# Kernel optimization log

Hardware: AMD Instinct MI355X
Metric: run time of the kernel (lower is better)

## Reference

```python
import jax, jax.numpy as jnp
import numpy as np

B = 16
NT, NH_, NW_, T_, H_, W_ = 4, 14, 14, 4, 1, 1
C = 768
NHEAD = 12
HD = C // NHEAD
SCALE = 1.0 / float(np.sqrt(HD))
TT = NT * T_            # 16 temporal slices
T2 = TT // 2            # 8 after even/odd split
HW = (NH_ * H_) * (NW_ * W_)  # 196 spatial tokens
TOKENS = NT * NH_ * NW_ * T_ * H_ * W_


def setup_inputs() -> dict:
    key = jax.random.key(0)
    ks = jax.random.split(key, 14)
    def lin(k, din, dout):
        return jax.random.normal(k, (din, dout), jnp.float32) * 0.02
    return {
        "x_in": jax.random.normal(ks[0], (B, TOKENS, C), jnp.float32),
        "Wq_d": lin(ks[1], C, C),      "bq_d": jnp.zeros((C,), jnp.float32),
        "Wkv_a": lin(ks[2], C, 2 * C), "bkv_a": jnp.zeros((2 * C,), jnp.float32),
        "Wq_a": lin(ks[3], C, C),      "bq_a": jnp.zeros((C,), jnp.float32),
        "Wkv_d": lin(ks[4], C, 2 * C), "bkv_d": jnp.zeros((2 * C,), jnp.float32),
        "Wp_d": lin(ks[5], C, C),      "bp_d": jnp.zeros((C,), jnp.float32),
        "Wp_a": lin(ks[6], C, C),      "bp_a": jnp.zeros((C,), jnp.float32),
    }


def _cross_attn(q_x, kv_x, Wq, bq, Wkv, bkv):
    # q_x, kv_x: (b, t, hw, c)
    b, t, hw, c = q_x.shape
    q = (q_x @ Wq + bq).reshape(b, t, hw, NHEAD, HD)
    kv = (kv_x @ Wkv + bkv).reshape(b, t, hw, 2, NHEAD, HD)
    k, v = kv[..., 0, :, :], kv[..., 1, :, :]
    s = jnp.einsum('btqhd,btkhd->bthqk', q, k) * SCALE
    p = jax.nn.softmax(s, axis=-1)
    o = jnp.einsum('bthqk,btkhd->btqhd', p, v)
    return o.reshape(b, t, hw, c)


def reference(x_in, Wq_d, bq_d, Wkv_a, bkv_a, Wq_a, bq_a, Wkv_d, bkv_d,
              Wp_d, bp_d, Wp_a, bp_a):
    b = x_in.shape[0]
    # einops: b (nt nh nw t h w) c -> b (nt t) (nh h) (nw w) c
    x = x_in.reshape(b, NT, NH_, NW_, T_, H_, W_, C)
    x = x.transpose(0, 1, 4, 2, 5, 3, 6, 7).reshape(b, TT, NH_ * H_, NW_ * W_, C)
    x_skip = x                                   # (b, TT, h, w, c)
    x = x.reshape(b, TT, HW, C)                  # (b, TT, hw, c)
    x_a = x[:, 0::2]                             # (b, T2, hw, c) approx
    x_d = x[:, 1::2]                             # (b, T2, hw, c) detail

    # detail cross-attends to approx, subtract-update
    _d = _cross_attn(x_d, x_a, Wq_d, bq_d, Wkv_a, bkv_a)
    _d = jax.nn.gelu(_d @ Wp_d + bp_d, approximate=False)
    x_d = x_d - _d
    # approx cross-attends to updated detail, add-update
    _a = _cross_attn(x_a, x_d, Wq_a, bq_a, Wkv_d, bkv_d)
    _a = jax.nn.gelu(_a @ Wp_a + bp_a, approximate=False)
    x_a = x_a + _a

    # relaxed_constrain: pooled-skip minus channel-mean of x_a
    xs = x_skip.reshape(b, TT, HW, C)
    pooled = xs.reshape(b, T2, 2, HW, C).mean(axis=2)   # avg_pool2d (2,1)
    pool_a = pooled.mean(axis=-1) - x_a.mean(axis=-1)   # (b, T2, hw)

    # SSL=False: mean over channels, keepdim (torch layout b,1,t,hw)
    x_d_out = x_d.mean(axis=-1)[:, None, :, :]          # (b, 1, T2, hw)
    return (pool_a, x_d_out)
```

## Files before the change

kernel.cpp:

```cpp
#include <hip/hip_runtime.h>

typedef __bf16 bf16;
typedef __attribute__((ext_vector_type(8))) __bf16 bf16x8;
typedef __attribute__((ext_vector_type(4))) __bf16 bf16x4;
typedef __attribute__((ext_vector_type(2))) __bf16 bf16x2;
typedef __attribute__((ext_vector_type(4))) float f32x4;
typedef __attribute__((ext_vector_type(4))) unsigned int u32x4;

#define TOKENS 3136
#define CC 768
#define S196 196
#define M_ROWS 25088
#define BATCH 16

__device__ __forceinline__ float bf2f(bf16 x) { return (float)x; }
__device__ __forceinline__ bf16 f2bf(float x) { return (bf16)x; }

__device__ __forceinline__ float gelu_exact(float x) {
    return 0.5f * x * (1.0f + erff(x * 0.70710678118654752f));
}

__device__ __forceinline__ unsigned int packbf(float a, float b) {
    bf16x2 v; v[0] = (bf16)a; v[1] = (bf16)b;
    return __builtin_bit_cast(unsigned int, v);
}

#define GLOAD_LDS16(gp, lp) \
    __builtin_amdgcn_global_load_lds((const __attribute__((address_space(1))) void*)(gp), \
                                     (__attribute__((address_space(3))) void*)(lp), 16, 0, 0)

__global__ __launch_bounds__(256)
void transpose_w(const float* __restrict__ W, bf16* __restrict__ Wt, int K, int N)
{
    __shared__ float tle[32][33];
    int k0 = blockIdx.x * 32, n0 = blockIdx.y * 32;
    int tx = threadIdx.x & 31, ty = threadIdx.x >> 5;
    for (int r = ty; r < 32; r += 8)
        tle[r][tx] = W[(long)(k0 + r) * N + n0 + tx];
    __syncthreads();
    for (int r = ty; r < 32; r += 8)
        Wt[(long)(n0 + r) * K + k0 + tx] = f2bf(tle[tx][r]);
}

__global__ __launch_bounds__(256)
void conv_bias(const float* b0, const float* b1, const float* b2,
               const float* b3, const float* b4, const float* b5,
               bf16* __restrict__ dst)
{
    const float* srcs[6] = {b0, b1, b2, b3, b4, b5};
    const int sizes[6]   = {768, 1536, 768, 1536, 768, 768};
    const int offs[6]    = {0, 768, 2304, 3072, 4608, 5376};
    int which = blockIdx.x;
    const float* s = srcs[which];
    int n = sizes[which];
    bf16* d = dst + offs[which];
    for (int i = threadIdx.x; i < n; i += 256)
        d[i] = f2bf(s[i]);
}

__global__ __launch_bounds__(256)
void reorder_split(const float* __restrict__ x_in, bf16* __restrict__ xa,
                   bf16* __restrict__ xd)
{
    long idx = (long)blockIdx.x * 256 + threadIdx.x;
    const long total = (long)BATCH * 16 * S196 * 96;
    if (idx >= total) return;
    int  c8  = (int)(idx % 96) * 8;
    long row = idx / 96;
    int  s   = (int)(row % S196);
    long r2  = row / S196;
    int  tt  = (int)(r2 & 15);
    int  b   = (int)(r2 >> 4);
    int  nt  = tt >> 2, t = tt & 3;
    int  nh  = s / 14,  nw = s % 14;
    long src  = ((long)b * TOKENS + ((nt * 14 + nh) * 14 + nw) * 4 + t) * CC + c8;
    bf16* dst = (tt & 1) ? xd : xa;
    long doff = ((long)(b * 8 + (tt >> 1)) * S196 + s) * CC + c8;
    const float* sp = x_in + src;
    f32x4 a = *(const f32x4*)sp;
    f32x4 c = *(const f32x4*)(sp + 4);
    bf16x8 v;
    v[0] = f2bf(a[0]); v[1] = f2bf(a[1]); v[2] = f2bf(a[2]); v[3] = f2bf(a[3]);
    v[4] = f2bf(c[0]); v[5] = f2bf(c[1]); v[6] = f2bf(c[2]); v[7] = f2bf(c[3]);
    *(bf16x8*)(dst + doff) = v;
}

__device__ __forceinline__ float row_sum768(const bf16* __restrict__ p, int lane)
{
    float s = 0.f;
    bf16x8 v = *(const bf16x8*)(p + lane * 8);
    #pragma unroll
    for (int j = 0; j < 8; ++j) s += bf2f(v[j]);
    if (lane < 32) {
        bf16x8 w = *(const bf16x8*)(p + 512 + lane * 8);
        #pragma unroll
        for (int j = 0; j < 8; ++j) s += bf2f(w[j]);
    }
    #pragma unroll
    for (int off = 32; off; off >>= 1) s += __shfl_xor(s, off, 64);
    return s;
}

__global__ __launch_bounds__(256)
void pool_ad(const bf16* __restrict__ xa, const bf16* __restrict__ xd,
             float* __restrict__ pool0)
{
    int id = blockIdx.x * 4 + (threadIdx.x >> 6);
    int lane = threadIdx.x & 63;
    float sa = row_sum768(xa + (long)id * CC, lane);
    float sd = row_sum768(xd + (long)id * CC, lane);
    if (lane == 0) pool0[id] = (sa + sd) * (0.5f / 768.0f);
}

__global__ __launch_bounds__(256)
void out_final(const bf16* __restrict__ xa, const bf16* __restrict__ xd,
               const float* __restrict__ pool0, float* __restrict__ out)
{
    int id = blockIdx.x * 4 + (threadIdx.x >> 6);
    int lane = threadIdx.x & 63;
    float sa = row_sum768(xa + (long)id * CC, lane);
    float sd = row_sum768(xd + (long)id * CC, lane);
    if (lane == 0) {
        out[id]          = pool0[id] - sa * (1.0f / 768.0f);
        out[M_ROWS + id] = sd * (1.0f / 768.0f);
    }
}

template<int EPI>
__global__ __launch_bounds__(256)
void gemm_bt128(const bf16* __restrict__ A, const bf16* __restrict__ Bt,
                const bf16* __restrict__ bias, const bf16* __restrict__ res,
                bf16* __restrict__ C, int ldc, int K, int mTiles, int nTiles)
{
    constexpr int BM = 128, BK = 32;
    __shared__ alignas(16) bf16 sA[BM * BK];
    __shared__ alignas(16) bf16 sB[BM * BK];
    const int tid  = threadIdx.x;
    const int lane = tid & 63, wave = tid >> 6;
    const int wm   = wave >> 1, wn = wave & 1;
    const int quad = lane >> 4, l16 = lane & 15;

    const int GM = 16;
    int pid   = blockIdx.x;
    int group = GM * nTiles;
    int gid   = pid / group;
    int rem   = pid - gid * group;
    int first = gid * GM;
    int gm    = (mTiles - first < GM) ? (mTiles - first) : GM;
    int bm    = first + rem % gm;
    int bn    = rem / gm;

    const long m0 = (long)bm * BM;
    const long n0 = (long)bn * BM;

    f32x4 acc[4][4] = {};

    for (int kt = 0; kt < K; kt += BK) {
        if (kt) __syncthreads();
        #pragma unroll
        for (int c = 0; c < 2; ++c) {
            int ci = (wave * 2 + c) * 64 + lane;
            int r  = ci >> 2, kc = ci & 3;
            const bf16* ga = A  + (m0 + r) * K + kt + kc * 8;
            const bf16* gb = Bt + (n0 + r) * K + kt + kc * 8;
            bf16* la = sA + (wave * 2 + c) * 512;
            bf16* lb = sB + (wave * 2 + c) * 512;
            GLOAD_LDS16(ga, la);
            GLOAD_LDS16(gb, lb);
        }
        __syncthreads();

        bf16x8 af[4], bfr[4];
        #pragma unroll
        for (int mi = 0; mi < 4; ++mi)
            af[mi] = *(const bf16x8*)(sA + (wm * 64 + mi * 16 + l16) * BK + quad * 8);
        #pragma unroll
        for (int ni = 0; ni < 4; ++ni)
            bfr[ni] = *(const bf16x8*)(sB + (wn * 64 + ni * 16 + l16) * BK + quad * 8);
        #pragma unroll
        for (int mi = 0; mi < 4; ++mi)
            #pragma unroll
            for (int ni = 0; ni < 4; ++ni)
                acc[mi][ni] = __builtin_amdgcn_mfma_f32_16x16x32_bf16(af[mi], bfr[ni], acc[mi][ni], 0, 0, 0);
    }

    #pragma unroll
    for (int mi = 0; mi < 4; ++mi) {
        #pragma unroll
        for (int ni = 0; ni < 4; ++ni) {
            int mg = (int)m0 + wm * 64 + mi * 16 + quad * 4;
            int ng = (int)n0 + wn * 64 + ni * 16 + l16;
            float bn_ = bf2f(bias[ng]);
            #pragma unroll
            for (int r = 0; r < 4; ++r) {
                float x = acc[mi][ni][r] + bn_;
                long off = (long)(mg + r) * ldc + ng;
                if (EPI == 0)      C[off] = f2bf(x);
                else if (EPI == 1) C[off] = f2bf(bf2f(res[off]) - gelu_exact(x));
                else               C[off] = f2bf(bf2f(res[off]) + gelu_exact(x));
            }
        }
    }
}

template<int EPI>
__global__ __launch_bounds__(512, 2)
void gemm_bt256(const bf16* __restrict__ A, const bf16* __restrict__ Bt,
                const bf16* __restrict__ bias, const bf16* __restrict__ res,
                bf16* __restrict__ C, int ldc, int mTiles, int nTiles)
{
    constexpr int K = 768, NKT = 12;
    __shared__ alignas(16) bf16 sA[4][8192];
    __shared__ alignas(16) bf16 sB[4][8192];
    const int tid  = threadIdx.x;
    const int lane = tid & 63, wave = tid >> 6;
    const int wm   = wave >> 2, wn = wave & 3;
    const int quad = lane >> 4, l16 = lane & 15;

    int nwg  = (int)gridDim.x;
    int orig = (int)blockIdx.x;
    int q8 = nwg >> 3, r8 = nwg & 7, xcd = orig & 7;
    int pid = (xcd < r8 ? xcd * (q8 + 1) : r8 * (q8 + 1) + (xcd - r8) * q8)
              + (orig >> 3);

    const int GM = 8;
    int group = GM * nTiles;
    int gid   = pid / group;
    int rem   = pid - gid * group;
    int first = gid * GM;
    int gm    = (mTiles - first < GM) ? (mTiles - first) : GM;
    int bm    = first + rem % gm;
    int bn    = rem / gm;

    const long m0 = (long)bm * 256;
    const long n0 = (long)bn * 256;

    const int lh  = l16 >> 1;
    const int px  = ((l16 & 1) << 2) | quad;
    const int pxl = (px ^ lh) * 8;
    const int aoffA = (wm * 64 + lh) * 64 + pxl;
    const int aoffB = (wn * 32 + lh) * 64 + pxl;

    const int  cg  = (tid & 7) ^ ((tid >> 3) & 7);
    const int  rr  = ((tid >> 3) << 1) + (cg >> 2);
    const long soA0 = (long)rr * K + (cg & 3) * 8;
    const long soA1 = (long)(128 + rr) * K + (cg & 3) * 8;
    const int  ldd0 = wave * 512, ldd1 = 4096 + wave * 512;
    const bf16* Ab = A  + m0 * K;
    const bf16* Bb = Bt + n0 * K;

    f32x4 acc[8][4] = {};

    #define STG_A(slot, koff) do { \
        GLOAD_LDS16(Ab + (koff) + soA0, &sA[slot][ldd0]); \
        GLOAD_LDS16(Ab + (koff) + soA1, &sA[slot][ldd1]); } while (0)
    #define STG_B(slot, koff) do { \
        GLOAD_LDS16(Bb + (koff) + soA0, &sB[slot][ldd0]); \
        GLOAD_LDS16(Bb + (koff) + soA1, &sB[slot][ldd1]); } while (0)

    STG_A(0, 0);  STG_B(0, 0);
    STG_A(1, 32); STG_B(1, 32);
    STG_A(2, 64); STG_B(2, 64);
    asm volatile("s_waitcnt vmcnt(8)" ::: "memory");
    __builtin_amdgcn_s_barrier();

    #define MFMA16(H) do { \
        __builtin_amdgcn_s_setprio(1); \
        _Pragma("unroll") \
        for (int mf = 0; mf < 4; ++mf) \
            _Pragma("unroll") \
            for (int nf = 0; nf < 4; ++nf) \
                acc[(H)*4 + mf][nf] = __builtin_amdgcn_mfma_f32_16x16x32_bf16( \
                    a[mf], b[nf], acc[(H)*4 + mf][nf], 0, 0, 0); \
        __builtin_amdgcn_s_setprio(0); } while (0)

    #pragma unroll 2
    for (int t = 0; t < NKT; ++t) {
        const int sl0 = (2 * t) & 3;
        const int sl1 = (2 * t + 1) & 3;
        const int slN = (2 * t + 3) & 3;
        bf16x8 a[4], b[4];

        #pragma unroll
        for (int mf = 0; mf < 4; ++mf) a[mf] = *(const bf16x8*)(&sA[sl0][mf * 512 + aoffA]);
        #pragma unroll
        for (int nf = 0; nf < 4; ++nf) b[nf] = *(const bf16x8*)(&sB[sl0][nf * 512 + aoffB]);
        if (t + 1 < NKT) STG_A(slN, (t + 1) * 64 + 32);
        __builtin_amdgcn_s_barrier();
        MFMA16(0);
        __builtin_amdgcn_s_barrier();

        #pragma unroll
        for (int mf = 0; mf < 4; ++mf) a[mf] = *(const bf16x8*)(&sA[sl0][2048 + mf * 512 + aoffA]);
        if (t + 1 < NKT) STG_B(slN, (t + 1) * 64 + 32);
        __builtin_amdgcn_s_barrier();
        MFMA16(1);
        if (t + 1 < NKT) asm volatile("s_waitcnt vmcnt(8)" ::: "memory");
        else             asm volatile("s_waitcnt vmcnt(0)" ::: "memory");
        __builtin_amdgcn_s_barrier();

        #pragma unroll
        for (int mf = 0; mf < 4; ++mf) a[mf] = *(const bf16x8*)(&sA[sl1][mf * 512 + aoffA]);
        #pragma unroll
        for (int nf = 0; nf < 4; ++nf) b[nf] = *(const bf16x8*)(&sB[sl1][nf * 512 + aoffB]);
        if (t + 2 < NKT) STG_A(sl0, (t + 2) * 64);
        __builtin_amdgcn_s_barrier();
        MFMA16(0);
        __builtin_amdgcn_s_barrier();

        #pragma unroll
        for (int mf = 0; mf < 4; ++mf) a[mf] = *(const bf16x8*)(&sA[sl1][2048 + mf * 512 + aoffA]);
        if (t + 2 < NKT) STG_B(sl0, (t + 2) * 64);
        __builtin_amdgcn_s_barrier();
        MFMA16(1);
        if      (t + 2 < NKT) asm volatile("s_waitcnt vmcnt(8)" ::: "memory");
        else if (t + 1 < NKT) asm volatile("s_waitcnt vmcnt(4)" ::: "memory");
        __builtin_amdgcn_s_barrier();
    }
    #undef STG_A
    #undef STG_B
    #undef MFMA16

    #pragma unroll
    for (int mf = 0; mf < 8; ++mf) {
        #pragma unroll
        for (int nf = 0; nf < 4; ++nf) {
            int mg = (int)m0 + wm * 128 + mf * 16 + quad * 4;
            int ng = (int)n0 + wn * 64 + nf * 16 + l16;
            float bn_ = bf2f(bias[ng]);
            #pragma unroll
            for (int r = 0; r < 4; ++r) {
                float x = acc[mf][nf][r] + bn_;
                long off = (long)(mg + r) * ldc + ng;
                if (EPI == 0)      C[off] = f2bf(x);
                else if (EPI == 1) C[off] = f2bf(bf2f(res[off]) - gelu_exact(x));
                else               C[off] = f2bf(bf2f(res[off]) + gelu_exact(x));
            }
        }
    }
}

#define KSTR 72
#define VSTR 264

__global__ __launch_bounds__(256)
void attn_mfma(const bf16* __restrict__ Q, int ldq,
               const bf16* __restrict__ KV, int ldkv,
               bf16* __restrict__ O)
{
    const int h  = blockIdx.x;
    const int bj = blockIdx.y;
    __shared__ alignas(16) bf16 Ks[208 * KSTR];
    __shared__ alignas(16) bf16 Vt[64 * VSTR];
    const int tid = threadIdx.x, lane = tid & 63, wave = tid >> 6;
    const int quad = lane >> 4, l16 = lane & 15;

    const bf16* qg = Q  + (long)bj * S196 * ldq  + h * 64;
    const bf16* kg = KV + (long)bj * S196 * ldkv + h * 64;
    const bf16* vg = kg + CC;

    for (int i = tid; i < 208 * 8; i += 256) {
        int r = i >> 3, c8 = (i & 7) * 8;
        bf16x8 v = {};
        if (r < S196) v = *(const bf16x8*)(kg + (long)r * ldkv + c8);
        *(bf16x8*)(Ks + r * KSTR + c8) = v;
    }
    for (int i = tid; i < 256 * 8; i += 256) {
        int g   = i >> 6;
        int c8  = (g & 7) * 8;
        int tok = (g >> 3) * 64 + (i & 63);
        bf16x8 v = {};
        if (tok < S196) v = *(const bf16x8*)(vg + (long)tok * ldkv + c8);
        #pragma unroll
        for (int j = 0; j < 8; ++j)
            Vt[(c8 + j) * VSTR + tok] = v[j];
    }
    __syncthreads();

    for (int qt = wave; qt < 13; qt += 4) {
        int qrow = qt * 16 + l16; if (qrow > 195) qrow = 195;
        const bf16* qrp = qg + (long)qrow * ldq + quad * 8;
        bf16x8 qf0 = *(const bf16x8*)(qrp);
        bf16x8 qf1 = *(const bf16x8*)(qrp + 32);

        f32x4 st[13];
        #pragma unroll
        for (int rt = 0; rt < 13; ++rt) st[rt] = (f32x4){0.f, 0.f, 0.f, 0.f};
        #pragma unroll
        for (int rt = 0; rt < 13; ++rt) {
            const bf16* kb = Ks + (rt * 16 + l16) * KSTR + quad * 8;
            bf16x8 kf0 = *(const bf16x8*)(kb);
            bf16x8 kf1 = *(const bf16x8*)(kb + 32);
            st[rt] = __builtin_amdgcn_mfma_f32_16x16x32_bf16(kf0, qf0, st[rt], 0, 0, 0);
            st[rt] = __builtin_amdgcn_mfma_f32_16x16x32_bf16(kf1, qf1, st[rt], 0, 0, 0);
        }

        const float SC = 0.125f;
        #pragma unroll
        for (int rt = 0; rt < 13; ++rt) {
            st[rt][0] *= SC; st[rt][1] *= SC; st[rt][2] *= SC; st[rt][3] *= SC;
        }
        if (quad != 0)
            st[12] = (f32x4){-1e30f, -1e30f, -1e30f, -1e30f};

        float m = -1e30f;
        #pragma unroll
        for (int rt = 0; rt < 13; ++rt)
            m = fmaxf(m, fmaxf(fmaxf(st[rt][0], st[rt][1]), fmaxf(st[rt][2], st[rt][3])));
        m = fmaxf(m, __shfl_xor(m, 16, 64));
        m = fmaxf(m, __shfl_xor(m, 32, 64));
        float sum = 0.f;
        #pragma unroll
        for (int rt = 0; rt < 13; ++rt) {
            st[rt][0] = __expf(st[rt][0] - m);
            st[rt][1] = __expf(st[rt][1] - m);
            st[rt][2] = __expf(st[rt][2] - m);
            st[rt][3] = __expf(st[rt][3] - m);
            sum += st[rt][0] + st[rt][1] + st[rt][2] + st[rt][3];
        }
        sum += __shfl_xor(sum, 16, 64);
        sum += __shfl_xor(sum, 32, 64);
        float inv = 1.0f / sum;

        unsigned int pk[13][2];
        #pragma unroll
        for (int rt = 0; rt < 13; ++rt) {
            pk[rt][0] = packbf(st[rt][0] * inv, st[rt][1] * inv);
            pk[rt][1] = packbf(st[rt][2] * inv, st[rt][3] * inv);
        }

        f32x4 ot[4];
        #pragma unroll
        for (int dt = 0; dt < 4; ++dt) ot[dt] = (f32x4){0.f, 0.f, 0.f, 0.f};
        #pragma unroll
        for (int c = 0; c < 7; ++c) {
            u32x4 fp;
            #pragma unroll
            for (int jp = 0; jp < 4; ++jp) {
                int jh = jp >> 1, rp = jp & 1;
                int srcb = ((((quad & 1) << 1) + jh) << 6) | (l16 << 2);
                int a = __builtin_amdgcn_ds_bpermute(srcb, (int)pk[2 * c][rp]);
                int b = (c < 6) ? __builtin_amdgcn_ds_bpermute(srcb, (int)pk[2 * c + 1][rp]) : 0;
                fp[jp] = (quad >> 1) ? (unsigned int)b : (unsigned int)a;
            }
            bf16x8 pB = __builtin_bit_cast(bf16x8, fp);
            #pragma unroll
            for (int dt = 0; dt < 4; ++dt) {
                bf16x8 vf = *(const bf16x8*)(Vt + (dt * 16 + l16) * VSTR + c * 32 + quad * 8);
                ot[dt] = __builtin_amdgcn_mfma_f32_16x16x32_bf16(vf, pB, ot[dt], 0, 0, 0);
            }
        }

        int token = qt * 16 + l16;
        if (token < S196) {
            bf16* op = O + ((long)bj * S196 + token) * CC + h * 64 + quad * 4;
            #pragma unroll
            for (int dt = 0; dt < 4; ++dt) {
                bf16x4 v;
                v[0] = f2bf(ot[dt][0]); v[1] = f2bf(ot[dt][1]);
                v[2] = f2bf(ot[dt][2]); v[3] = f2bf(ot[dt][3]);
                *(bf16x4*)(op + dt * 16) = v;
            }
        }
    }
}

extern "C" void kernel_launch(void* const* d_in, const int* in_sizes, int n_in,
                              void* d_out, int out_size, void* d_ws, size_t ws_size,
                              hipStream_t stream)
{
    const float* x_in  = (const float*)d_in[0];
    const float* Wq_d  = (const float*)d_in[1];
    const float* bq_d  = (const float*)d_in[2];
    const float* Wkv_a = (const float*)d_in[3];
    const float* bkv_a = (const float*)d_in[4];
    const float* Wq_a  = (const float*)d_in[5];
    const float* bq_a  = (const float*)d_in[6];
    const float* Wkv_d = (const float*)d_in[7];
    const float* bkv_d = (const float*)d_in[8];
    const float* Wp_d  = (const float*)d_in[9];
    const float* bp_d  = (const float*)d_in[10];
    const float* Wp_a  = (const float*)d_in[11];
    const float* bp_a  = (const float*)d_in[12];
    float* out = (float*)d_out;

    char* w = (char*)d_ws;
    auto alloc = [&](size_t elems) {
        bf16* p = (bf16*)w;
        w += ((elems * 2 + 255) / 256) * 256;
        return p;
    };
    bf16* biasAll = alloc(6144);
    bf16* WtQd  = alloc((size_t)768 * 768);
    bf16* WtACat= alloc((size_t)2304 * 768);
    bf16* WtKd  = alloc((size_t)1536 * 768);
    bf16* WtPd  = alloc((size_t)768 * 768);
    bf16* WtPa  = alloc((size_t)768 * 768);
    bf16* xa    = alloc((size_t)M_ROWS * 768);
    bf16* xd    = alloc((size_t)M_ROWS * 768);
    bf16* Qb    = alloc((size_t)M_ROWS * 768);
    bf16* QKVa  = alloc((size_t)M_ROWS * 2304);
    bf16* Ob    = alloc((size_t)M_ROWS * 768);
    float* pool0 = (float*)w; w += ((size_t)M_ROWS * 4 + 255) / 256 * 256;

    dim3 blk(256);
    dim3 blk512(512);
    transpose_w<<<dim3(24, 24), blk, 0, stream>>>(Wq_d,  WtQd, 768, 768);
    transpose_w<<<dim3(24, 48), blk, 0, stream>>>(Wkv_a, WtACat, 768, 1536);
    transpose_w<<<dim3(24, 24), blk, 0, stream>>>(Wq_a,  WtACat + (size_t)1536 * 768, 768, 768);
    transpose_w<<<dim3(24, 48), blk, 0, stream>>>(Wkv_d, WtKd, 768, 1536);
    transpose_w<<<dim3(24, 24), blk, 0, stream>>>(Wp_d,  WtPd, 768, 768);
    transpose_w<<<dim3(24, 24), blk, 0, stream>>>(Wp_a,  WtPa, 768, 768);
    conv_bias<<<dim3(6), blk, 0, stream>>>(bq_d, bkv_a, bq_a, bkv_d, bp_d, bp_a, biasAll);

    long total_chunks = (long)BATCH * 16 * S196 * 96;
    int  rblocks = (int)((total_chunks + 255) / 256);
    reorder_split<<<rblocks, blk, 0, stream>>>(x_in, xa, xd);
    pool_ad<<<M_ROWS / 4, blk, 0, stream>>>(xa, xd, pool0);

    const bf16* Bq_d   = biasAll;
    const bf16* Bkva_qa= biasAll + 768;
    const bf16* Bkv_d  = biasAll + 3072;
    const bf16* Bp_d   = biasAll + 4608;
    const bf16* Bp_a   = biasAll + 5376;

    gemm_bt128<0><<<dim3(196 * 6), blk, 0, stream>>>(xd, WtQd, Bq_d, nullptr, Qb, 768, 768, 196, 6);
    gemm_bt256<0><<<dim3(98 * 9), blk512, 0, stream>>>(xa, WtACat, Bkva_qa, nullptr, QKVa, 2304, 98, 9);
    attn_mfma<<<dim3(12, 128), blk, 0, stream>>>(Qb, 768, QKVa, 2304, Ob);
    gemm_bt128<1><<<dim3(196 * 6), blk, 0, stream>>>(Ob, WtPd, Bp_d, xd, xd, 768, 768, 196, 6);

    gemm_bt128<0><<<dim3(196 * 12), blk, 0, stream>>>(xd, WtKd, Bkv_d, nullptr, QKVa, 2304, 768, 196, 12);
    attn_mfma<<<dim3(12, 128), blk, 0, stream>>>(QKVa + 1536, 2304, QKVa, 2304, Ob);
    gemm_bt128<2><<<dim3(196 * 6), blk, 0, stream>>>(Ob, WtPa, Bp_a, xa, xa, 768, 768, 196, 6);

    out_final<<<M_ROWS / 4, blk, 0, stream>>>(xa, xd, pool0, out);
}
```

Baseline: 864.0 us.

## Fuse channel row-sums into GEMM epilogues, remap blocks per XCD, merge transposes

Adds per-row channel sums to the output-projection GEMM epilogues, reduced with wave shuffles and atomicAdd. This replaces the final out_final pass that re-read xa and xd, and the updated xa is no longer written back. The six weight-transpose launches become one kernel, and the gemm_bt128 block index is remapped so consecutive tiles land on the same XCD for L2 locality. The cost is float atomics, so summation order is no longer deterministic, plus extra zero-init stores in pool_ad.

Measured after the change: 886.5 us. 1.03x slower.

```diff
diff --git a/kernel.cpp b/kernel.cpp
--- a/kernel.cpp
+++ b/kernel.cpp
@@ -30,10 +30,29 @@
                                      (__attribute__((address_space(3))) void*)(lp), 16, 0, 0)
 
 __global__ __launch_bounds__(256)
-void transpose_w(const float* __restrict__ W, bf16* __restrict__ Wt, int K, int N)
-{
+void transpose_all(const float* W0, const float* W1, const float* W2,
+                   const float* W3, const float* W4, const float* W5,
+                   bf16* D0, bf16* D1, bf16* D2, bf16* D3, bf16* D4, bf16* D5)
+{
+    const int base[7] = {0, 576, 1728, 2304, 3456, 4032, 4608};
+    const float* srcs[6] = {W0, W1, W2, W3, W4, W5};
+    bf16*        dsts[6] = {D0, D1, D2, D3, D4, D5};
+    const int    Ns[6]   = {768, 1536, 768, 1536, 768, 768};
+
+    int bid = blockIdx.x;
+    int which = 0;
+    #pragma unroll
+    for (int j = 0; j < 6; ++j) if (bid >= base[j + 1]) which = j + 1;
+    int t  = bid - base[which];
+    int N  = Ns[which];
+    const float* W  = srcs[which];
+    bf16*        Wt = dsts[which];
+    const int K = 768;
+
+    int kx = t % 24, ny = t / 24;
+    int k0 = kx * 32, n0 = ny * 32;
+
     __shared__ float tle[32][33];
-    int k0 = blockIdx.x * 32, n0 = blockIdx.y * 32;
     int tx = threadIdx.x & 31, ty = threadIdx.x >> 5;
     for (int r = ty; r < 32; r += 8)
         tle[r][tx] = W[(long)(k0 + r) * N + n0 + tx];
@@ -103,26 +122,28 @@
 
 __global__ __launch_bounds__(256)
 void pool_ad(const bf16* __restrict__ xa, const bf16* __restrict__ xd,
-             float* __restrict__ pool0)
-{
-    int id = blockIdx.x * 4 + (threadIdx.x >> 6);
-    int lane = threadIdx.x & 63;
-    float sa = row_sum768(xa + (long)id * CC, lane);
-    float sd = row_sum768(xd + (long)id * CC, lane);
-    if (lane == 0) pool0[id] = (sa + sd) * (0.5f / 768.0f);
-}
-
-__global__ __launch_bounds__(256)
-void out_final(const bf16* __restrict__ xa, const bf16* __restrict__ xd,
-               const float* __restrict__ pool0, float* __restrict__ out)
+             float* __restrict__ pool0, float* __restrict__ rs_a,
+             float* __restrict__ rs_d)
 {
     int id = blockIdx.x * 4 + (threadIdx.x >> 6);
     int lane = threadIdx.x & 63;
     float sa = row_sum768(xa + (long)id * CC, lane);
     float sd = row_sum768(xd + (long)id * CC, lane);
     if (lane == 0) {
-        out[id]          = pool0[id] - sa * (1.0f / 768.0f);
-        out[M_ROWS + id] = sd * (1.0f / 768.0f);
+        pool0[id] = (sa + sd) * (0.5f / 768.0f);
+        rs_a[id] = 0.f;
+        rs_d[id] = 0.f;
+    }
+}
+
+__global__ __launch_bounds__(256)
+void out_combine(const float* __restrict__ pool0, const float* __restrict__ rs_a,
+                 const float* __restrict__ rs_d, float* __restrict__ out)
+{
+    int id = blockIdx.x * 256 + threadIdx.x;
+    if (id < M_ROWS) {
+        out[id]          = pool0[id] - rs_a[id] * (1.0f / 768.0f);
+        out[M_ROWS + id] = rs_d[id] * (1.0f / 768.0f);
     }
 }
 
@@ -130,7 +151,8 @@
 __global__ __launch_bounds__(256)
 void gemm_bt128(const bf16* __restrict__ A, const bf16* __restrict__ Bt,
                 const bf16* __restrict__ bias, const bf16* __restrict__ res,
-                bf16* __restrict__ C, int ldc, int K, int mTiles, int nTiles)
+                bf16* __restrict__ C, float* __restrict__ rowsum,
+                int ldc, int K, int mTiles, int nTiles)
 {
     constexpr int BM = 128, BK = 32;
     __shared__ alignas(16) bf16 sA[BM * BK];
@@ -140,8 +162,13 @@
     const int wm   = wave >> 1, wn = wave & 1;
     const int quad = lane >> 4, l16 = lane & 15;
 
+    int nwg  = (int)gridDim.x;
+    int orig = (int)blockIdx.x;
+    int q8 = nwg >> 3, r8 = nwg & 7, xcd = orig & 7;
+    int pid = (xcd < r8 ? xcd * (q8 + 1) : r8 * (q8 + 1) + (xcd - r8) * q8)
+              + (orig >> 3);
+
     const int GM = 16;
-    int pid   = blockIdx.x;
     int group = GM * nTiles;
     int gid   = pid / group;
     int rem   = pid - gid * group;
@@ -184,6 +211,14 @@
                 acc[mi][ni] = __builtin_amdgcn_mfma_f32_16x16x32_bf16(af[mi], bfr[ni], acc[mi][ni], 0, 0, 0);
     }
 
+    float rsum[4][4];
+    if (EPI != 0) {
+        #pragma unroll
+        for (int mi = 0; mi < 4; ++mi)
+            #pragma unroll
+            for (int r = 0; r < 4; ++r) rsum[mi][r] = 0.f;
+    }
+
     #pragma unroll
     for (int mi = 0; mi < 4; ++mi) {
         #pragma unroll
@@ -195,9 +230,34 @@
             for (int r = 0; r < 4; ++r) {
                 float x = acc[mi][ni][r] + bn_;
                 long off = (long)(mg + r) * ldc + ng;
-                if (EPI == 0)      C[off] = f2bf(x);
-                else if (EPI == 1) C[off] = f2bf(bf2f(res[off]) - gelu_exact(x));
-                else               C[off] = f2bf(bf2f(res[off]) + gelu_exact(x));
+                if (EPI == 0) {
+                    C[off] = f2bf(x);
+                } else if (EPI == 1) {
+                    bf16 v = f2bf(bf2f(res[off]) - gelu_exact(x));
+                    C[off] = v;
+                    rsum[mi][r] += bf2f(v);
+                } else {
+                    bf16 v = f2bf(bf2f(res[off]) + gelu_exact(x));
+                    rsum[mi][r] += bf2f(v);
+                }
+            }
+        }
+    }
+
+    if (EPI != 0) {
+        #pragma unroll
+        for (int mi = 0; mi < 4; ++mi) {
+            #pragma unroll
+            for (int r = 0; r < 4; ++r) {
+                float v = rsum[mi][r];
+                v += __shfl_xor(v, 1, 64);
+                v += __shfl_xor(v, 2, 64);
+                v += __shfl_xor(v, 4, 64);
+                v += __shfl_xor(v, 8, 64);
+                if (l16 == 0) {
+                    int mg = (int)m0 + wm * 64 + mi * 16 + quad * 4 + r;
+                    atomicAdd(&rowsum[mg], v);
+                }
             }
         }
     }
@@ -502,21 +562,21 @@
     bf16* QKVa  = alloc((size_t)M_ROWS * 2304);
     bf16* Ob    = alloc((size_t)M_ROWS * 768);
     float* pool0 = (float*)w; w += ((size_t)M_ROWS * 4 + 255) / 256 * 256;
+    float* rs_a  = (float*)w; w += ((size_t)M_ROWS * 4 + 255) / 256 * 256;
+    float* rs_d  = (float*)w; w += ((size_t)M_ROWS * 4 + 255) / 256 * 256;
 
     dim3 blk(256);
     dim3 blk512(512);
-    transpose_w<<<dim3(24, 24), blk, 0, stream>>>(Wq_d,  WtQd, 768, 768);
-    transpose_w<<<dim3(24, 48), blk, 0, stream>>>(Wkv_a, WtACat, 768, 1536);
-    transpose_w<<<dim3(24, 24), blk, 0, stream>>>(Wq_a,  WtACat + (size_t)1536 * 768, 768, 768);
-    transpose_w<<<dim3(24, 48), blk, 0, stream>>>(Wkv_d, WtKd, 768, 1536);
-    transpose_w<<<dim3(24, 24), blk, 0, stream>>>(Wp_d,  WtPd, 768, 768);
-    transpose_w<<<dim3(24, 24), blk, 0, stream>>>(Wp_a,  WtPa, 768, 768);
+
+    transpose_all<<<dim3(4608), blk, 0, stream>>>(
+        Wq_d, Wkv_a, Wq_a, Wkv_d, Wp_d, Wp_a,
+        WtQd, WtACat, WtACat + (size_t)1536 * 768, WtKd, WtPd, WtPa);
     conv_bias<<<dim3(6), blk, 0, stream>>>(bq_d, bkv_a, bq_a, bkv_d, bp_d, bp_a, biasAll);
 
     long total_chunks = (long)BATCH * 16 * S196 * 96;
     int  rblocks = (int)((total_chunks + 255) / 256);
     reorder_split<<<rblocks, blk, 0, stream>>>(x_in, xa, xd);
-    pool_ad<<<M_ROWS / 4, blk, 0, stream>>>(xa, xd, pool0);
+    pool_ad<<<M_ROWS / 4, blk, 0, stream>>>(xa, xd, pool0, rs_a, rs_d);
 
     const bf16* Bq_d   = biasAll;
     const bf16* Bkva_qa= biasAll + 768;
@@ -524,14 +584,14 @@
     const bf16* Bp_d   = biasAll + 4608;
     const bf16* Bp_a   = biasAll + 5376;
 
-    gemm_bt128<0><<<dim3(196 * 6), blk, 0, stream>>>(xd, WtQd, Bq_d, nullptr, Qb, 768, 768, 196, 6);
+    gemm_bt128<0><<<dim3(196 * 6), blk, 0, stream>>>(xd, WtQd, Bq_d, nullptr, Qb, nullptr, 768, 768, 196, 6);
     gemm_bt256<0><<<dim3(98 * 9), blk512, 0, stream>>>(xa, WtACat, Bkva_qa, nullptr, QKVa, 2304, 98, 9);
     attn_mfma<<<dim3(12, 128), blk, 0, stream>>>(Qb, 768, QKVa, 2304, Ob);
-    gemm_bt128<1><<<dim3(196 * 6), blk, 0, stream>>>(Ob, WtPd, Bp_d, xd, xd, 768, 768, 196, 6);
-
-    gemm_bt128<0><<<dim3(196 * 12), blk, 0, stream>>>(xd, WtKd, Bkv_d, nullptr, QKVa, 2304, 768, 196, 12);
+    gemm_bt128<1><<<dim3(196 * 6), blk, 0, stream>>>(Ob, WtPd, Bp_d, xd, xd, rs_d, 768, 768, 196, 6);
+
+    gemm_bt128<0><<<dim3(196 * 12), blk, 0, stream>>>(xd, WtKd, Bkv_d, nullptr, QKVa, nullptr, 2304, 768, 196, 12);
     attn_mfma<<<dim3(12, 128), blk, 0, stream>>>(QKVa + 1536, 2304, QKVa, 2304, Ob);
-    gemm_bt128<2><<<dim3(196 * 6), blk, 0, stream>>>(Ob, WtPa, Bp_a, xa, xa, 768, 768, 196, 6);
-
-    out_final<<<M_ROWS / 4, blk, 0, stream>>>(xa, xd, pool0, out);
-}
+    gemm_bt128<2><<<dim3(196 * 6), blk, 0, stream>>>(Ob, WtPa, Bp_a, xa, nullptr, rs_a, 768, 768, 196, 6);
+
+    out_combine<<<dim3((M_ROWS + 255) / 256), blk, 0, stream>>>(pool0, rs_a, rs_d, out);
+}
```
